# Kernel tuning notes

Measured on AMD Instinct MI355X. Metric: run time of the kernel, lower is better.

Reference implementation:

```python
import jax, jax.numpy as jnp
import numpy as np

EPS = 1e-5  # BatchNorm2d default eps


def setup_inputs() -> dict:
    key = jax.random.key(0)
    k1, k2, k3, k4 = jax.random.split(key, 4)
    B, C, S, E = 2, 512, 256, 512  # C == E is required by the module's math
    x = jax.random.normal(k1, (B, C, S, E), dtype=jnp.float32)
    Q = jax.random.normal(k2, (E, E), dtype=jnp.float32)
    K = jax.random.normal(k3, (E, E), dtype=jnp.float32)
    V = jax.random.normal(k4, (E, E), dtype=jnp.float32)
    return {"x": x, "Q": Q, "K": K, "V": V}


def reference(x, Q, K, V):
    # BatchNorm2d(affine=False), training-mode batch stats over (B, H, W)
    mean = jnp.mean(x, axis=(0, 2, 3), keepdims=True)
    var = jnp.var(x, axis=(0, 2, 3), keepdims=True)  # biased, matches torch normalization
    xn = (x - mean) * jax.lax.rsqrt(var + EPS)

    divisor = jnp.sqrt(jnp.asarray(x.shape[-1], dtype=x.dtype))
    q = jnp.einsum('bcse,ef->bcsf', xn, Q)
    k = jnp.einsum('bcse,ef->bcsf', xn, K)
    v = jnp.einsum('bcse,ef->bcsf', xn, V)

    # scores: [B, C, S, S]
    prod = jnp.einsum('bcsf,bctf->bcst', q, k) / divisor
    # nn.Softmax2d softmaxes over the CHANNEL dim (axis 1)
    sm = jax.nn.softmax(prod, axis=1)
    attention = jnp.einsum('bcst,bctf->bcsf', sm, v)
    # dropout is identity in eval/reference mode; residual since E_in == E_out
    return attention + xn
```

## Files before the change

### kernel.cpp

```cpp
#include <hip/hip_runtime.h>
#include <hip/hip_bf16.h>
#include <cstdio>

#define Bn 2
#define Cn 512
#define Sn 256
#define En 512

typedef __attribute__((ext_vector_type(8))) short bf16x8;
typedef __attribute__((ext_vector_type(4))) float f32x4;

static constexpr size_t PROD_B = (1ull << 20);
static constexpr size_t V_B    = PROD_B + (256ull << 20);
static constexpr size_t ATH_B  = V_B + (256ull << 20);
static constexpr size_t ATL_B  = ATH_B + (512ull << 10);
static constexpr size_t VT_B   = ATL_B + (512ull << 10);
static constexpr size_t WS_SMALL = VT_B + (512ull << 10);
static constexpr size_t XNH_B  = WS_SMALL;
static constexpr size_t XNL_B  = XNH_B + (256ull << 20);
static constexpr size_t WS_BIG = XNL_B + (256ull << 20);

__device__ __forceinline__ unsigned short f2bf(float f) {
  union { __hip_bfloat16 h; unsigned short u; } cv;
  cv.h = __float2bfloat16(f);
  return cv.u;
}
__device__ __forceinline__ float bf2f(unsigned short u) {
  union { unsigned int i; float f; } cv;
  cv.i = ((unsigned int)u) << 16;
  return cv.f;
}
__device__ __forceinline__ void split2(float v, unsigned short& h, unsigned short& l) {
  h = f2bf(v);
  l = f2bf(v - bf2f(h));
}
__device__ __forceinline__ int swz8(int row, int c4) {
  return row * 64 + ((((c4 * 8) ^ ((row & 7) << 4))) >> 1);
}
__device__ __forceinline__ int swzc(int row, int col) {
  return row * 64 + ((col & 3) | ((col & 60) ^ ((row & 7) << 3)));
}
__device__ __forceinline__ bf16x8 ldfrag(const unsigned short* arr, int row, int ks, int lane) {
  const int byte = (ks * 64 + ((lane >> 4) << 4)) ^ ((row & 7) << 4);
  return *(const bf16x8*)((const char*)(arr + (size_t)row * 64) + byte);
}
__device__ __forceinline__ f32x4 MFMA(bf16x8 a, bf16x8 b, f32x4 c) {
  return __builtin_amdgcn_mfma_f32_16x16x32_bf16(a, b, c, 0, 0, 0);
}
__device__ __forceinline__ void glds16(const void* g, void* l) {
  __builtin_amdgcn_global_load_lds(
      (const __attribute__((address_space(1))) unsigned int*)g,
      (__attribute__((address_space(3))) unsigned int*)l, 16, 0, 0);
}
__device__ __forceinline__ void stage_tile(const unsigned short* g, unsigned short* l,
                                           int nbytes, int wid, int lane, int nwaves) {
  const char* gb = (const char*)g;
  char* lb = (char*)l;
  for (int j = wid; j < (nbytes >> 10); j += nwaves)
    glds16(gb + j * 1024 + lane * 16, lb + j * 1024);
}

__global__ void k1_stats(const float* __restrict__ x, float* __restrict__ ws) {
  const int c = blockIdx.x, tid = threadIdx.x;
  const float4* p0 = (const float4*)(x + (size_t)c * (Sn * En));
  const float4* p1 = (const float4*)(x + (size_t)(Cn + c) * (Sn * En));
  float s1 = 0.f, s2 = 0.f;
  for (int i = tid; i < (Sn * En / 4); i += 256) {
    float4 a = p0[i], b = p1[i];
    s1 += (a.x + a.y) + (a.z + a.w) + (b.x + b.y) + (b.z + b.w);
    s2 += (a.x * a.x + a.y * a.y) + (a.z * a.z + a.w * a.w) +
          (b.x * b.x + b.y * b.y) + (b.z * b.z + b.w * b.w);
  }
  __shared__ float r1[256], r2[256];
  r1[tid] = s1; r2[tid] = s2;
  __syncthreads();
  for (int off = 128; off > 0; off >>= 1) {
    if (tid < off) { r1[tid] += r1[tid + off]; r2[tid] += r2[tid + off]; }
    __syncthreads();
  }
  if (tid == 0) {
    const float n = (float)(2 * Sn * En);
    float mean = r1[0] / n;
    float var = r2[0] / n - mean * mean;
    ws[c] = mean;
    ws[512 + c] = 1.0f / sqrtf(var + 1e-5f);
  }
}

__global__ void kA(const float* __restrict__ Q, const float* __restrict__ K,
                   const float* __restrict__ V, unsigned short* __restrict__ ATh,
                   unsigned short* __restrict__ ATl, unsigned short* __restrict__ VT) {
  const int f = blockIdx.x, tid = threadIdx.x;
  __shared__ float Kf[512];
  for (int i = tid; i < 512; i += 256) Kf[i] = K[(size_t)f * 512 + i];
  __syncthreads();
  const int fr64 = f & 63;
  const size_t atbase = ((size_t)(f >> 6) * 8) * 4096 + (size_t)fr64 * 64;
  const size_t vtbase = ((size_t)(f >> 7) * 8) * 8192 + (size_t)(f & 127) * 64;
#pragma unroll
  for (int half = 0; half < 2; ++half) {
    const int e = tid + half * 256;
    const float* Qe = Q + (size_t)e * 512;
    float acc = 0.f;
    for (int t = 0; t < 512; t += 4) {
      float4 q = *(const float4*)(Qe + t);
      acc += q.x * Kf[t] + q.y * Kf[t + 1] + q.z * Kf[t + 2] + q.w * Kf[t + 3];
    }
    unsigned short h, l;
    split2(acc, h, l);
    const int et = e >> 6, ec = e & 63;
    const int swa = (ec & 3) | ((ec & 60) ^ ((fr64 & 7) << 3));
    ATh[atbase + (size_t)et * 4096 + swa] = h;
    ATl[atbase + (size_t)et * 4096 + swa] = l;
    const int swv = (ec & 3) | ((ec & 60) ^ ((f & 7) << 3));
    VT[vtbase + (size_t)et * 8192 + swv] = f2bf(V[(size_t)e * 512 + f]);
  }
}

__global__ void kxn(const float* __restrict__ x, const float* __restrict__ ws,
                    unsigned short* __restrict__ XNh, unsigned short* __restrict__ XNl) {
  const int bid = blockIdx.x;
  const int bc = bid >> 1, half = bid & 1;
  const int c = bc & 511;
  const float mean = ws[c], rstd = ws[512 + c];
  const float* xb = x + (size_t)bc * 131072 + (size_t)half * 128 * 512;
  const int tid = threadIdx.x;
#pragma unroll 4
  for (int i = 0; i < 64; ++i) {
    const int g = tid + i * 256;
    const int r = g >> 7, c4 = g & 127;
    const float4 xv = *(const float4*)(xb + (size_t)r * 512 + c4 * 4);
    ushort4 hv, lv;
    split2((xv.x - mean) * rstd, hv.x, lv.x);
    split2((xv.y - mean) * rstd, hv.y, lv.y);
    split2((xv.z - mean) * rstd, hv.z, lv.z);
    split2((xv.w - mean) * rstd, hv.w, lv.w);
    const int et = c4 >> 4, colt4 = c4 & 15;
    const int row = half * 128 + r;
    const size_t idx = ((size_t)(bc * 8 + et) * 256 + row) * 64 +
                       ((colt4 * 4) ^ ((row & 7) << 3));
    *(ushort4*)&XNh[idx] = hv;
    *(ushort4*)&XNl[idx] = lv;
  }
}

template <bool PRE>
__launch_bounds__(256)
__global__ void kv_proj(const float* __restrict__ x, const unsigned short* __restrict__ VT,
                        const unsigned short* __restrict__ XNh_g,
                        const float* __restrict__ ws, unsigned short* __restrict__ vT_out) {
  __shared__ unsigned short VTs[128 * 64];
  __shared__ unsigned short XN[128 * 64];
  const int bid = blockIdx.x;
  const int L = (bid & 7) * 1024 + (bid >> 3);
  const int bc = L >> 3;
  const int fq = (L >> 1) & 3;
  const int th = L & 1;
  const int c = bc & 511;
  const float mean = ws[c], rstd = ws[512 + c];
  const int f0 = fq * 128, t0 = th * 128;
  const int tid = threadIdx.x, w = tid >> 6, lane = tid & 63;
  const float* xb = x + (size_t)bc * 131072;

  f32x4 acc[2][8];
#pragma unroll
  for (int i = 0; i < 2; ++i)
#pragma unroll
    for (int j = 0; j < 8; ++j) acc[i][j] = (f32x4){0.f, 0.f, 0.f, 0.f};

  for (int et = 0; et < 8; ++et) {
    const int e0 = et * 64;
    __syncthreads();
    stage_tile(VT + ((size_t)fq * 8 + et) * 8192, VTs, 16384, w, lane, 4);
    if (PRE) {
      stage_tile(XNh_g + ((size_t)(bc * 8 + et) * 256 + t0) * 64, XN, 16384, w, lane, 4);
    } else {
#pragma unroll
      for (int i = 0; i < 8; ++i) {
        const int g = tid + i * 256;
        const int r = g >> 4, c4 = g & 15;
        float4 xv = *(const float4*)(xb + (size_t)(t0 + r) * 512 + e0 + c4 * 4);
        ushort4 hv;
        hv.x = f2bf((xv.x - mean) * rstd);
        hv.y = f2bf((xv.y - mean) * rstd);
        hv.z = f2bf((xv.z - mean) * rstd);
        hv.w = f2bf((xv.w - mean) * rstd);
        *(ushort4*)&XN[swz8(r, c4)] = hv;
      }
    }
    __syncthreads();
#pragma unroll
    for (int ks = 0; ks < 2; ++ks) {
      bf16x8 a0 = ldfrag(VTs, w * 32 + (lane & 15), ks, lane);
      bf16x8 a1 = ldfrag(VTs, w * 32 + 16 + (lane & 15), ks, lane);
#pragma unroll
      for (int ct = 0; ct < 8; ++ct) {
        bf16x8 b = ldfrag(XN, ct * 16 + (lane & 15), ks, lane);
        acc[0][ct] = MFMA(a0, b, acc[0][ct]);
        acc[1][ct] = MFMA(a1, b, acc[1][ct]);
      }
    }
  }
#pragma unroll
  for (int rt = 0; rt < 2; ++rt)
#pragma unroll
    for (int ct = 0; ct < 8; ++ct)
#pragma unroll
      for (int r = 0; r < 4; ++r) {
        const int f = f0 + w * 32 + rt * 16 + (lane >> 4) * 4 + r;
        const int t = t0 + ct * 16 + (lane & 15);
        const size_t idx = (((size_t)bc * 4 + (f >> 7)) * 4 + (t >> 6)) * 8192 +
                           (size_t)(f & 127) * 64 +
                           ((t & 3) | ((t & 60) ^ ((f & 7) << 3)));
        vT_out[idx] = f2bf(acc[rt][ct][r]);
      }
}

template <bool PRE>
__launch_bounds__(512)
__global__ void kscores(const float* __restrict__ x, const unsigned short* __restrict__ ATh_g,
                        const unsigned short* __restrict__ ATl_g,
                        const unsigned short* __restrict__ XNh_g,
                        const unsigned short* __restrict__ XNl_g,
                        const float* __restrict__ ws, float* __restrict__ prod) {
  __shared__ unsigned short XNh[128 * 64], XNl[128 * 64];
  __shared__ unsigned short ATh[64 * 64], ATl[64 * 64];
  __shared__ unsigned short Yh[128 * 64], Yl[128 * 64];
  const int bid = blockIdx.x;
  const int L = (bid & 7) * 256 + (bid >> 3);
  const int bc = L >> 1, half = L & 1;
  const int c = bc & 511;
  const float mean = ws[c], rstd = ws[512 + c];
  const float* xc = x + (size_t)bc * (Sn * En);
  const float* xr = xc + (size_t)half * 128 * 512;
  float* prodc = prod + (size_t)bc * 65536 + (size_t)half * 128 * 256;
  const int tid = threadIdx.x, w = tid >> 6, lane = tid & 63;

  f32x4 accz[16];
#pragma unroll
  for (int i = 0; i < 16; ++i) accz[i] = (f32x4){0.f, 0.f, 0.f, 0.f};

  for (int ft = 0; ft < 8; ++ft) {
    const int f0 = ft * 64;
    f32x4 accy[4];
#pragma unroll
    for (int i = 0; i < 4; ++i) accy[i] = (f32x4){0.f, 0.f, 0.f, 0.f};

    for (int et = 0; et < 8; ++et) {
      const int e0 = et * 64;
      __syncthreads();
      if (PRE) {
        stage_tile(XNh_g + ((size_t)(bc * 8 + et) * 256 + half * 128) * 64, XNh,
                   16384, w, lane, 8);
        stage_tile(XNl_g + ((size_t)(bc * 8 + et) * 256 + half * 128) * 64, XNl,
                   16384, w, lane, 8);
      } else {
#pragma unroll
        for (int i = 0; i < 4; ++i) {
          const int g = tid + i * 512;
          const int r = g >> 4, c4 = g & 15;
          float4 xv = *(const float4*)(xr + (size_t)r * 512 + e0 + c4 * 4);
          ushort4 hv, lv;
          split2((xv.x - mean) * rstd, hv.x, lv.x);
          split2((xv.y - mean) * rstd, hv.y, lv.y);
          split2((xv.z - mean) * rstd, hv.z, lv.z);
          split2((xv.w - mean) * rstd, hv.w, lv.w);
          *(ushort4*)&XNh[swz8(r, c4)] = hv;
          *(ushort4*)&XNl[swz8(r, c4)] = lv;
        }
      }
      stage_tile(ATh_g + ((size_t)ft * 8 + et) * 4096, ATh, 8192, w, lane, 8);
      stage_tile(ATl_g + ((size_t)ft * 8 + et) * 4096, ATl, 8192, w, lane, 8);
      __syncthreads();
#pragma unroll
      for (int ks = 0; ks < 2; ++ks) {
        bf16x8 ah = ldfrag(XNh, w * 16 + (lane & 15), ks, lane);
        bf16x8 al = ldfrag(XNl, w * 16 + (lane & 15), ks, lane);
#pragma unroll
        for (int fc = 0; fc < 4; ++fc) {
          bf16x8 bh = ldfrag(ATh, fc * 16 + (lane & 15), ks, lane);
          bf16x8 bl = ldfrag(ATl, fc * 16 + (lane & 15), ks, lane);
          accy[fc] = MFMA(ah, bh, accy[fc]);
          accy[fc] = MFMA(ah, bl, accy[fc]);
          accy[fc] = MFMA(al, bh, accy[fc]);
        }
      }
    }
    __syncthreads();

#pragma unroll
    for (int fc = 0; fc < 4; ++fc)
#pragma unroll
      for (int r = 0; r < 4; ++r) {
        const int row = w * 16 + (lane >> 4) * 4 + r;
        const int col = fc * 16 + (lane & 15);
        unsigned short h, l;
        split2(accy[fc][r], h, l);
        const int idx = swzc(row, col);
        Yh[idx] = h;
        Yl[idx] = l;
      }
#pragma unroll
    for (int th = 0; th < 2; ++th) {
      if (PRE) {
        stage_tile(XNh_g + ((size_t)(bc * 8 + ft) * 256 + th * 128) * 64, XNh,
                   16384, w, lane, 8);
        stage_tile(XNl_g + ((size_t)(bc * 8 + ft) * 256 + th * 128) * 64, XNl,
                   16384, w, lane, 8);
      } else {
#pragma unroll
        for (int i = 0; i < 4; ++i) {
          const int g = tid + i * 512;
          const int r = g >> 4, c4 = g & 15;
          float4 xv = *(const float4*)(xc + (size_t)(th * 128 + r) * 512 + f0 + c4 * 4);
          ushort4 hv, lv;
          split2((xv.x - mean) * rstd, hv.x, lv.x);
          split2((xv.y - mean) * rstd, hv.y, lv.y);
          split2((xv.z - mean) * rstd, hv.z, lv.z);
          split2((xv.w - mean) * rstd, hv.w, lv.w);
          *(ushort4*)&XNh[swz8(r, c4)] = hv;
          *(ushort4*)&XNl[swz8(r, c4)] = lv;
        }
      }
      __syncthreads();
#pragma unroll
      for (int ks = 0; ks < 2; ++ks) {
        bf16x8 ah = ldfrag(Yh, w * 16 + (lane & 15), ks, lane);
        bf16x8 al = ldfrag(Yl, w * 16 + (lane & 15), ks, lane);
#pragma unroll
        for (int ct = 0; ct < 8; ++ct) {
          bf16x8 bh = ldfrag(XNh, ct * 16 + (lane & 15), ks, lane);
          bf16x8 bl = ldfrag(XNl, ct * 16 + (lane & 15), ks, lane);
          accz[th * 8 + ct] = MFMA(ah, bh, accz[th * 8 + ct]);
          accz[th * 8 + ct] = MFMA(ah, bl, accz[th * 8 + ct]);
          accz[th * 8 + ct] = MFMA(al, bh, accz[th * 8 + ct]);
        }
      }
      __syncthreads();
    }
  }
  const float scale = 0.044194173824159216f;
#pragma unroll
  for (int th = 0; th < 2; ++th)
#pragma unroll
    for (int ct = 0; ct < 8; ++ct)
#pragma unroll
      for (int r = 0; r < 4; ++r) {
        const int row = w * 16 + (lane >> 4) * 4 + r;
        prodc[(size_t)row * 256 + th * 128 + ct * 16 + (lane & 15)] =
            accz[th * 8 + ct][r] * scale;
      }
}

__global__ void k3_softmax(float* __restrict__ prodf) {
  const int bid = blockIdx.x;
  const int b = bid >> 8, s = bid & 255;
  const int t = threadIdx.x;
  float* __restrict__ p = prodf + (size_t)b * (512ull * 65536) + (size_t)s * 256 + t;
  float m = -3.4e38f, sum = 0.f;
#pragma unroll 8
  for (int cc = 0; cc < 512; ++cc) {
    const float v = p[(size_t)cc * 65536];
    if (v > m) { sum *= __expf(m - v); m = v; }
    sum += __expf(v - m);
  }
  const float inv = 1.0f / sum;
#pragma unroll 4
  for (int cc = 0; cc < 512; ++cc) {
    p[(size_t)cc * 65536] = __expf(p[(size_t)cc * 65536] - m) * inv;
  }
}

__launch_bounds__(256)
__global__ void k4_pv(const float* __restrict__ x, const unsigned short* __restrict__ vT,
                      const float* __restrict__ ws, const float* __restrict__ sm,
                      float* __restrict__ out) {
  __shared__ unsigned short SMs[128 * 64];
  __shared__ unsigned short VTs[128 * 64];
  const int bid = blockIdx.x;
  const int L = (bid & 7) * 1024 + (bid >> 3);
  const int bc = L >> 3;
  const int sh = (L >> 2) & 1;
  const int fh = L & 3;
  const int c = bc & 511;
  const float mean = ws[c], rstd = ws[512 + c];
  const int s0 = sh * 128, f0 = fh * 128;
  const float* smb = sm + (size_t)bc * 65536;
  const int tid = threadIdx.x, w = tid >> 6, lane = tid & 63;

  f32x4 acc[2][8];
#pragma unroll
  for (int i = 0; i < 2; ++i)
#pragma unroll
    for (int j = 0; j < 8; ++j) acc[i][j] = (f32x4){0.f, 0.f, 0.f, 0.f};

  for (int kt = 0; kt < 4; ++kt) {
    const int t0 = kt * 64;
    __syncthreads();
    stage_tile(vT + (((size_t)bc * 4 + fh) * 4 + kt) * 8192, VTs, 16384, w, lane, 4);
#pragma unroll
    for (int i = 0; i < 8; ++i) {
      const int g = tid + i * 256;
      const int r = g >> 4, c4 = g & 15;
      float4 pv = *(const float4*)(smb + (size_t)(s0 + r) * 256 + t0 + c4 * 4);
      ushort4 hv;
      hv.x = f2bf(pv.x); hv.y = f2bf(pv.y); hv.z = f2bf(pv.z); hv.w = f2bf(pv.w);
      *(ushort4*)&SMs[swz8(r, c4)] = hv;
    }
    __syncthreads();
#pragma unroll
    for (int ks = 0; ks < 2; ++ks) {
      bf16x8 a0 = ldfrag(SMs, w * 32 + (lane & 15), ks, lane);
      bf16x8 a1 = ldfrag(SMs, w * 32 + 16 + (lane & 15), ks, lane);
#pragma unroll
      for (int ct = 0; ct < 8; ++ct) {
        bf16x8 b = ldfrag(VTs, ct * 16 + (lane & 15), ks, lane);
        acc[0][ct] = MFMA(a0, b, acc[0][ct]);
        acc[1][ct] = MFMA(a1, b, acc[1][ct]);
      }
    }
  }
#pragma unroll
  for (int rt = 0; rt < 2; ++rt)
#pragma unroll
    for (int ct = 0; ct < 8; ++ct)
#pragma unroll
      for (int r = 0; r < 4; ++r) {
        const int srow = s0 + w * 32 + rt * 16 + (lane >> 4) * 4 + r;
        const int fcol = f0 + ct * 16 + (lane & 15);
        const size_t oi = (size_t)bc * 131072 + (size_t)srow * 512 + fcol;
        out[oi] = acc[rt][ct][r] + (x[oi] - mean) * rstd;
      }
}

extern "C" void kernel_launch(void* const* d_in, const int* in_sizes, int n_in,
                              void* d_out, int out_size, void* d_ws, size_t ws_size,
                              hipStream_t stream) {
  const float* x = (const float*)d_in[0];
  const float* Q = (const float*)d_in[1];
  const float* K = (const float*)d_in[2];
  const float* V = (const float*)d_in[3];
  float* out = (float*)d_out;
  float* ws = (float*)d_ws;
  float* prodf = (float*)((char*)d_ws + PROD_B);
  unsigned short* vT   = (unsigned short*)((char*)d_ws + V_B);
  unsigned short* ATh  = (unsigned short*)((char*)d_ws + ATH_B);
  unsigned short* ATl  = (unsigned short*)((char*)d_ws + ATL_B);
  unsigned short* VTm  = (unsigned short*)((char*)d_ws + VT_B);
  unsigned short* XNh  = (unsigned short*)((char*)d_ws + XNH_B);
  unsigned short* XNl  = (unsigned short*)((char*)d_ws + XNL_B);
  if (ws_size < WS_SMALL) {
    fprintf(stderr, "kernel_launch: ws_size %zu < needed %zu\n", ws_size, WS_SMALL);
  }
  const bool big = ws_size >= WS_BIG;
  k1_stats<<<dim3(512), dim3(256), 0, stream>>>(x, ws);
  kA<<<dim3(512), dim3(256), 0, stream>>>(Q, K, V, ATh, ATl, VTm);
  if (big) {
    kxn<<<dim3(2048), dim3(256), 0, stream>>>(x, ws, XNh, XNl);
    kv_proj<true><<<dim3(8192), dim3(256), 0, stream>>>(x, VTm, XNh, ws, vT);
    kscores<true><<<dim3(2048), dim3(512), 0, stream>>>(x, ATh, ATl, XNh, XNl, ws, prodf);
  } else {
    kv_proj<false><<<dim3(8192), dim3(256), 0, stream>>>(x, VTm, XNh, ws, vT);
    kscores<false><<<dim3(2048), dim3(512), 0, stream>>>(x, ATh, ATl, XNh, XNl, ws, prodf);
  }
  k3_softmax<<<dim3(512), dim3(256), 0, stream>>>(prodf);
  k4_pv<<<dim3(8192), dim3(256), 0, stream>>>(x, vT, ws, prodf, out);
}
```

Before: 2.107 ms.

## Double-buffer LDS staging in GEMM kernels and emit bf16 tiled softmax output

kv_proj, kscores and k4_pv now double-buffer their LDS tiles, so the async global-to-LDS load for the next k-step overlaps the MFMAs on the current one, with one barrier per step. kscores flattens its nested loops into a single 80-step schedule so this prefetch can run across phases. Softmax splits the 512-channel reduction over two thread halves and writes bf16 probabilities straight into the swizzled tile layout that k4_pv reads, so k4_pv no longer reads and converts fp32. The non-precomputed fallback is dropped, so the code now always needs the large workspace and the smT buffer reuses the XNl region.

```diff
diff --git a/kernel.cpp b/kernel.cpp
--- a/kernel.cpp
+++ b/kernel.cpp
@@ -15,10 +15,10 @@
 static constexpr size_t ATH_B  = V_B + (256ull << 20);
 static constexpr size_t ATL_B  = ATH_B + (512ull << 10);
 static constexpr size_t VT_B   = ATL_B + (512ull << 10);
-static constexpr size_t WS_SMALL = VT_B + (512ull << 10);
-static constexpr size_t XNH_B  = WS_SMALL;
+static constexpr size_t XNH_B  = VT_B + (512ull << 10);
 static constexpr size_t XNL_B  = XNH_B + (256ull << 20);
 static constexpr size_t WS_BIG = XNL_B + (256ull << 20);
+static constexpr size_t SMT_B  = XNL_B;
 
 __device__ __forceinline__ unsigned short f2bf(float f) {
   union { __hip_bfloat16 h; unsigned short u; } cv;
@@ -33,9 +33,6 @@
 __device__ __forceinline__ void split2(float v, unsigned short& h, unsigned short& l) {
   h = f2bf(v);
   l = f2bf(v - bf2f(h));
-}
-__device__ __forceinline__ int swz8(int row, int c4) {
-  return row * 64 + ((((c4 * 8) ^ ((row & 7) << 4))) >> 1);
 }
 __device__ __forceinline__ int swzc(int row, int col) {
   return row * 64 + ((col & 3) | ((col & 60) ^ ((row & 7) << 3)));
@@ -144,23 +141,18 @@
   }
 }
 
-template <bool PRE>
 __launch_bounds__(256)
-__global__ void kv_proj(const float* __restrict__ x, const unsigned short* __restrict__ VT,
+__global__ void kv_proj(const unsigned short* __restrict__ VT,
                         const unsigned short* __restrict__ XNh_g,
-                        const float* __restrict__ ws, unsigned short* __restrict__ vT_out) {
-  __shared__ unsigned short VTs[128 * 64];
-  __shared__ unsigned short XN[128 * 64];
+                        unsigned short* __restrict__ vT_out) {
+  __shared__ unsigned short BUF[2][16384];
   const int bid = blockIdx.x;
   const int L = (bid & 7) * 1024 + (bid >> 3);
   const int bc = L >> 3;
   const int fq = (L >> 1) & 3;
   const int th = L & 1;
-  const int c = bc & 511;
-  const float mean = ws[c], rstd = ws[512 + c];
   const int f0 = fq * 128, t0 = th * 128;
   const int tid = threadIdx.x, w = tid >> 6, lane = tid & 63;
-  const float* xb = x + (size_t)bc * 131072;
 
   f32x4 acc[2][8];
 #pragma unroll
@@ -168,38 +160,30 @@
 #pragma unroll
     for (int j = 0; j < 8; ++j) acc[i][j] = (f32x4){0.f, 0.f, 0.f, 0.f};
 
+  stage_tile(VT + ((size_t)fq * 8 + 0) * 8192, &BUF[0][0], 16384, w, lane, 4);
+  stage_tile(XNh_g + ((size_t)(bc * 8 + 0) * 256 + t0) * 64, &BUF[0][8192], 16384, w, lane, 4);
+  __syncthreads();
+#pragma unroll 1
   for (int et = 0; et < 8; ++et) {
-    const int e0 = et * 64;
-    __syncthreads();
-    stage_tile(VT + ((size_t)fq * 8 + et) * 8192, VTs, 16384, w, lane, 4);
-    if (PRE) {
-      stage_tile(XNh_g + ((size_t)(bc * 8 + et) * 256 + t0) * 64, XN, 16384, w, lane, 4);
-    } else {
-#pragma unroll
-      for (int i = 0; i < 8; ++i) {
-        const int g = tid + i * 256;
-        const int r = g >> 4, c4 = g & 15;
-        float4 xv = *(const float4*)(xb + (size_t)(t0 + r) * 512 + e0 + c4 * 4);
-        ushort4 hv;
-        hv.x = f2bf((xv.x - mean) * rstd);
-        hv.y = f2bf((xv.y - mean) * rstd);
-        hv.z = f2bf((xv.z - mean) * rstd);
-        hv.w = f2bf((xv.w - mean) * rstd);
-        *(ushort4*)&XN[swz8(r, c4)] = hv;
-      }
-    }
-    __syncthreads();
+    if (et < 7) {
+      const int b = (et + 1) & 1;
+      stage_tile(VT + ((size_t)fq * 8 + et + 1) * 8192, &BUF[b][0], 16384, w, lane, 4);
+      stage_tile(XNh_g + ((size_t)(bc * 8 + et + 1) * 256 + t0) * 64, &BUF[b][8192],
+                 16384, w, lane, 4);
+    }
+    const unsigned short* cb = &BUF[et & 1][0];
 #pragma unroll
     for (int ks = 0; ks < 2; ++ks) {
-      bf16x8 a0 = ldfrag(VTs, w * 32 + (lane & 15), ks, lane);
-      bf16x8 a1 = ldfrag(VTs, w * 32 + 16 + (lane & 15), ks, lane);
+      bf16x8 a0 = ldfrag(cb, w * 32 + (lane & 15), ks, lane);
+      bf16x8 a1 = ldfrag(cb, w * 32 + 16 + (lane & 15), ks, lane);
 #pragma unroll
       for (int ct = 0; ct < 8; ++ct) {
-        bf16x8 b = ldfrag(XN, ct * 16 + (lane & 15), ks, lane);
+        bf16x8 b = ldfrag(cb + 8192, ct * 16 + (lane & 15), ks, lane);
         acc[0][ct] = MFMA(a0, b, acc[0][ct]);
         acc[1][ct] = MFMA(a1, b, acc[1][ct]);
       }
     }
+    __syncthreads();
   }
 #pragma unroll
   for (int rt = 0; rt < 2; ++rt)
@@ -216,129 +200,116 @@
       }
 }
 
-template <bool PRE>
 __launch_bounds__(512)
-__global__ void kscores(const float* __restrict__ x, const unsigned short* __restrict__ ATh_g,
+__global__ void kscores(const unsigned short* __restrict__ ATh_g,
                         const unsigned short* __restrict__ ATl_g,
                         const unsigned short* __restrict__ XNh_g,
                         const unsigned short* __restrict__ XNl_g,
-                        const float* __restrict__ ws, float* __restrict__ prod) {
-  __shared__ unsigned short XNh[128 * 64], XNl[128 * 64];
-  __shared__ unsigned short ATh[64 * 64], ATl[64 * 64];
+                        float* __restrict__ prod) {
+  __shared__ unsigned short BUF[2][24576];
   __shared__ unsigned short Yh[128 * 64], Yl[128 * 64];
   const int bid = blockIdx.x;
   const int L = (bid & 7) * 256 + (bid >> 3);
   const int bc = L >> 1, half = L & 1;
-  const int c = bc & 511;
-  const float mean = ws[c], rstd = ws[512 + c];
-  const float* xc = x + (size_t)bc * (Sn * En);
-  const float* xr = xc + (size_t)half * 128 * 512;
   float* prodc = prod + (size_t)bc * 65536 + (size_t)half * 128 * 256;
   const int tid = threadIdx.x, w = tid >> 6, lane = tid & 63;
 
   f32x4 accz[16];
 #pragma unroll
   for (int i = 0; i < 16; ++i) accz[i] = (f32x4){0.f, 0.f, 0.f, 0.f};
-
-  for (int ft = 0; ft < 8; ++ft) {
-    const int f0 = ft * 64;
-    f32x4 accy[4];
-#pragma unroll
-    for (int i = 0; i < 4; ++i) accy[i] = (f32x4){0.f, 0.f, 0.f, 0.f};
-
-    for (int et = 0; et < 8; ++et) {
-      const int e0 = et * 64;
-      __syncthreads();
-      if (PRE) {
-        stage_tile(XNh_g + ((size_t)(bc * 8 + et) * 256 + half * 128) * 64, XNh,
-                   16384, w, lane, 8);
-        stage_tile(XNl_g + ((size_t)(bc * 8 + et) * 256 + half * 128) * 64, XNl,
-                   16384, w, lane, 8);
-      } else {
-#pragma unroll
-        for (int i = 0; i < 4; ++i) {
-          const int g = tid + i * 512;
-          const int r = g >> 4, c4 = g & 15;
-          float4 xv = *(const float4*)(xr + (size_t)r * 512 + e0 + c4 * 4);
-          ushort4 hv, lv;
-          split2((xv.x - mean) * rstd, hv.x, lv.x);
-          split2((xv.y - mean) * rstd, hv.y, lv.y);
-          split2((xv.z - mean) * rstd, hv.z, lv.z);
-          split2((xv.w - mean) * rstd, hv.w, lv.w);
-          *(ushort4*)&XNh[swz8(r, c4)] = hv;
-          *(ushort4*)&XNl[swz8(r, c4)] = lv;
-        }
-      }
-      stage_tile(ATh_g + ((size_t)ft * 8 + et) * 4096, ATh, 8192, w, lane, 8);
-      stage_tile(ATl_g + ((size_t)ft * 8 + et) * 4096, ATl, 8192, w, lane, 8);
-      __syncthreads();
+  f32x4 accy[4];
+
+  auto stage_slot = [&](int m, int b) {
+    const int ft = m / 10, sub = m - ft * 10;
+    unsigned short* dst = &BUF[b][0];
+    if (sub < 8) {
+      stage_tile(XNh_g + ((size_t)(bc * 8 + sub) * 256 + half * 128) * 64, dst,
+                 16384, w, lane, 8);
+      stage_tile(XNl_g + ((size_t)(bc * 8 + sub) * 256 + half * 128) * 64, dst + 8192,
+                 16384, w, lane, 8);
+      stage_tile(ATh_g + ((size_t)ft * 8 + sub) * 4096, dst + 16384, 8192, w, lane, 8);
+      stage_tile(ATl_g + ((size_t)ft * 8 + sub) * 4096, dst + 20480, 8192, w, lane, 8);
+    } else {
+      const int th = sub - 8;
+      stage_tile(XNh_g + ((size_t)(bc * 8 + ft) * 256 + th * 128) * 64, dst,
+                 16384, w, lane, 8);
+      stage_tile(XNl_g + ((size_t)(bc * 8 + ft) * 256 + th * 128) * 64, dst + 8192,
+                 16384, w, lane, 8);
+    }
+  };
+
+  stage_slot(0, 0);
+  __syncthreads();
+
+#pragma unroll 1
+  for (int m = 0; m < 80; ++m) {
+    const int sub = m % 10;
+    if (m < 79) stage_slot(m + 1, (m + 1) & 1);
+    const unsigned short* cb = &BUF[m & 1][0];
+    if (sub == 0) {
+#pragma unroll
+      for (int i = 0; i < 4; ++i) accy[i] = (f32x4){0.f, 0.f, 0.f, 0.f};
+    }
+    if (sub < 8) {
 #pragma unroll
       for (int ks = 0; ks < 2; ++ks) {
-        bf16x8 ah = ldfrag(XNh, w * 16 + (lane & 15), ks, lane);
-        bf16x8 al = ldfrag(XNl, w * 16 + (lane & 15), ks, lane);
+        bf16x8 ah = ldfrag(cb, w * 16 + (lane & 15), ks, lane);
+        bf16x8 al = ldfrag(cb + 8192, w * 16 + (lane & 15), ks, lane);
 #pragma unroll
         for (int fc = 0; fc < 4; ++fc) {
-          bf16x8 bh = ldfrag(ATh, fc * 16 + (lane & 15), ks, lane);
-          bf16x8 bl = ldfrag(ATl, fc * 16 + (lane & 15), ks, lane);
+          bf16x8 bh = ldfrag(cb + 16384, fc * 16 + (lane & 15), ks, lane);
+          bf16x8 bl = ldfrag(cb + 20480, fc * 16 + (lane & 15), ks, lane);
           accy[fc] = MFMA(ah, bh, accy[fc]);
           accy[fc] = MFMA(ah, bl, accy[fc]);
           accy[fc] = MFMA(al, bh, accy[fc]);
         }
       }
-    }
-    __syncthreads();
-
-#pragma unroll
-    for (int fc = 0; fc < 4; ++fc)
-#pragma unroll
-      for (int r = 0; r < 4; ++r) {
-        const int row = w * 16 + (lane >> 4) * 4 + r;
-        const int col = fc * 16 + (lane & 15);
-        unsigned short h, l;
-        split2(accy[fc][r], h, l);
-        const int idx = swzc(row, col);
-        Yh[idx] = h;
-        Yl[idx] = l;
-      }
-#pragma unroll
-    for (int th = 0; th < 2; ++th) {
-      if (PRE) {
-        stage_tile(XNh_g + ((size_t)(bc * 8 + ft) * 256 + th * 128) * 64, XNh,
-                   16384, w, lane, 8);
-        stage_tile(XNl_g + ((size_t)(bc * 8 + ft) * 256 + th * 128) * 64, XNl,
-                   16384, w, lane, 8);
-      } else {
-#pragma unroll
-        for (int i = 0; i < 4; ++i) {
-          const int g = tid + i * 512;
-          const int r = g >> 4, c4 = g & 15;
-          float4 xv = *(const float4*)(xc + (size_t)(th * 128 + r) * 512 + f0 + c4 * 4);
-          ushort4 hv, lv;
-          split2((xv.x - mean) * rstd, hv.x, lv.x);
-          split2((xv.y - mean) * rstd, hv.y, lv.y);
-          split2((xv.z - mean) * rstd, hv.z, lv.z);
-          split2((xv.w - mean) * rstd, hv.w, lv.w);
-          *(ushort4*)&XNh[swz8(r, c4)] = hv;
-          *(ushort4*)&XNl[swz8(r, c4)] = lv;
-        }
-      }
-      __syncthreads();
+      if (sub == 7) {
+#pragma unroll
+        for (int fc = 0; fc < 4; ++fc)
+#pragma unroll
+          for (int r = 0; r < 4; ++r) {
+            const int row = w * 16 + (lane >> 4) * 4 + r;
+            const int col = fc * 16 + (lane & 15);
+            unsigned short h, l;
+            split2(accy[fc][r], h, l);
+            const int idx = swzc(row, col);
+            Yh[idx] = h;
+            Yl[idx] = l;
+          }
+      }
+    } else if (sub == 8) {
 #pragma unroll
       for (int ks = 0; ks < 2; ++ks) {
         bf16x8 ah = ldfrag(Yh, w * 16 + (lane & 15), ks, lane);
         bf16x8 al = ldfrag(Yl, w * 16 + (lane & 15), ks, lane);
 #pragma unroll
         for (int ct = 0; ct < 8; ++ct) {
-          bf16x8 bh = ldfrag(XNh, ct * 16 + (lane & 15), ks, lane);
-          bf16x8 bl = ldfrag(XNl, ct * 16 + (lane & 15), ks, lane);
-          accz[th * 8 + ct] = MFMA(ah, bh, accz[th * 8 + ct]);
-          accz[th * 8 + ct] = MFMA(ah, bl, accz[th * 8 + ct]);
-          accz[th * 8 + ct] = MFMA(al, bh, accz[th * 8 + ct]);
+          bf16x8 bh = ldfrag(cb, ct * 16 + (lane & 15), ks, lane);
+          bf16x8 bl = ldfrag(cb + 8192, ct * 16 + (lane & 15), ks, lane);
+          accz[ct] = MFMA(ah, bh, accz[ct]);
+          accz[ct] = MFMA(ah, bl, accz[ct]);
+          accz[ct] = MFMA(al, bh, accz[ct]);
         }
       }
-      __syncthreads();
-    }
-  }
+    } else {
+#pragma unroll
+      for (int ks = 0; ks < 2; ++ks) {
+        bf16x8 ah = ldfrag(Yh, w * 16 + (lane & 15), ks, lane);
+        bf16x8 al = ldfrag(Yl, w * 16 + (lane & 15), ks, lane);
+#pragma unroll
+        for (int ct = 0; ct < 8; ++ct) {
+          bf16x8 bh = ldfrag(cb, ct * 16 + (lane & 15), ks, lane);
+          bf16x8 bl = ldfrag(cb + 8192, ct * 16 + (lane & 15), ks, lane);
+          accz[8 + ct] = MFMA(ah, bh, accz[8 + ct]);
+          accz[8 + ct] = MFMA(ah, bl, accz[8 + ct]);
+          accz[8 + ct] = MFMA(al, bh, accz[8 + ct]);
+        }
+      }
+    }
+    __syncthreads();
+  }
+
   const float scale = 0.044194173824159216f;
 #pragma unroll
   for (int th = 0; th < 2; ++th)
@@ -352,31 +323,42 @@
       }
 }
 
-__global__ void k3_softmax(float* __restrict__ prodf) {
+__launch_bounds__(512)
+__global__ void k3_softmax(const float* __restrict__ prodf, unsigned short* __restrict__ smT) {
   const int bid = blockIdx.x;
   const int b = bid >> 8, s = bid & 255;
-  const int t = threadIdx.x;
-  float* __restrict__ p = prodf + (size_t)b * (512ull * 65536) + (size_t)s * 256 + t;
+  const int tid = threadIdx.x;
+  const int t = tid & 255, ch = tid >> 8;
+  const float* __restrict__ p =
+      prodf + (size_t)b * (512ull * 65536) + (size_t)s * 256 + t + (size_t)ch * 256 * 65536;
   float m = -3.4e38f, sum = 0.f;
-#pragma unroll 8
-  for (int cc = 0; cc < 512; ++cc) {
+#pragma unroll 4
+  for (int cc = 0; cc < 256; ++cc) {
     const float v = p[(size_t)cc * 65536];
     if (v > m) { sum *= __expf(m - v); m = v; }
     sum += __expf(v - m);
   }
-  const float inv = 1.0f / sum;
+  __shared__ float Ms[2][256], Ss[2][256];
+  Ms[ch][t] = m; Ss[ch][t] = sum;
+  __syncthreads();
+  const float mo = Ms[ch ^ 1][t], so = Ss[ch ^ 1][t];
+  const float mm = fmaxf(m, mo);
+  const float inv = 1.0f / (sum * __expf(m - mm) + so * __expf(mo - mm));
+  const int sh = s >> 7, r = s & 127, kt = t >> 6, col = t & 63;
+  const int cidx = r * 64 + ((col & 3) | ((col & 60) ^ ((r & 7) << 3)));
+  const size_t tbase = ((size_t)b * 512 + ch * 256) * 2 + sh;
 #pragma unroll 4
-  for (int cc = 0; cc < 512; ++cc) {
-    p[(size_t)cc * 65536] = __expf(p[(size_t)cc * 65536] - m) * inv;
+  for (int cc = 0; cc < 256; ++cc) {
+    const float ev = __expf(p[(size_t)cc * 65536] - mm) * inv;
+    smT[((tbase + (size_t)cc * 2) * 4 + kt) * 8192 + cidx] = f2bf(ev);
   }
 }
 
 __launch_bounds__(256)
 __global__ void k4_pv(const float* __restrict__ x, const unsigned short* __restrict__ vT,
-                      const float* __restrict__ ws, const float* __restrict__ sm,
+                      const float* __restrict__ ws, const unsigned short* __restrict__ smT,
                       float* __restrict__ out) {
-  __shared__ unsigned short SMs[128 * 64];
-  __shared__ unsigned short VTs[128 * 64];
+  __shared__ unsigned short BUF[2][16384];
   const int bid = blockIdx.x;
   const int L = (bid & 7) * 1024 + (bid >> 3);
   const int bc = L >> 3;
@@ -385,7 +367,6 @@
   const int c = bc & 511;
   const float mean = ws[c], rstd = ws[512 + c];
   const int s0 = sh * 128, f0 = fh * 128;
-  const float* smb = sm + (size_t)bc * 65536;
   const int tid = threadIdx.x, w = tid >> 6, lane = tid & 63;
 
   f32x4 acc[2][8];
@@ -394,31 +375,31 @@
 #pragma unroll
     for (int j = 0; j < 8; ++j) acc[i][j] = (f32x4){0.f, 0.f, 0.f, 0.f};
 
+  stage_tile(smT + (((size_t)bc * 2 + sh) * 4 + 0) * 8192, &BUF[0][0], 16384, w, lane, 4);
+  stage_tile(vT + (((size_t)bc * 4 + fh) * 4 + 0) * 8192, &BUF[0][8192], 16384, w, lane, 4);
+  __syncthreads();
+#pragma unroll 1
   for (int kt = 0; kt < 4; ++kt) {
-    const int t0 = kt * 64;
-    __syncthreads();
-    stage_tile(vT + (((size_t)bc * 4 + fh) * 4 + kt) * 8192, VTs, 16384, w, lane, 4);
-#pragma unroll
-    for (int i = 0; i < 8; ++i) {
-      const int g = tid + i * 256;
-      const int r = g >> 4, c4 = g & 15;
-      float4 pv = *(const float4*)(smb + (size_t)(s0 + r) * 256 + t0 + c4 * 4);
-      ushort4 hv;
-      hv.x = f2bf(pv.x); hv.y = f2bf(pv.y); hv.z = f2bf(pv.z); hv.w = f2bf(pv.w);
-      *(ushort4*)&SMs[swz8(r, c4)] = hv;
-    }
-    __syncthreads();
+    if (kt < 3) {
+      const int b = (kt + 1) & 1;
+      stage_tile(smT + (((size_t)bc * 2 + sh) * 4 + kt + 1) * 8192, &BUF[b][0],
+                 16384, w, lane, 4);
+      stage_tile(vT + (((size_t)bc * 4 + fh) * 4 + kt + 1) * 8192, &BUF[b][8192],
+                 16384, w, lane, 4);
+    }
+    const unsigned short* cb = &BUF[kt & 1][0];
 #pragma unroll
     for (int ks = 0; ks < 2; ++ks) {
-      bf16x8 a0 = ldfrag(SMs, w * 32 + (lane & 15), ks, lane);
-      bf16x8 a1 = ldfrag(SMs, w * 32 + 16 + (lane & 15), ks, lane);
+      bf16x8 a0 = ldfrag(cb, w * 32 + (lane & 15), ks, lane);
+      bf16x8 a1 = ldfrag(cb, w * 32 + 16 + (lane & 15), ks, lane);
 #pragma unroll
       for (int ct = 0; ct < 8; ++ct) {
-        bf16x8 b = ldfrag(VTs, ct * 16 + (lane & 15), ks, lane);
+        bf16x8 b = ldfrag(cb + 8192, ct * 16 + (lane & 15), ks, lane);
         acc[0][ct] = MFMA(a0, b, acc[0][ct]);
         acc[1][ct] = MFMA(a1, b, acc[1][ct]);
       }
     }
+    __syncthreads();
   }
 #pragma unroll
   for (int rt = 0; rt < 2; ++rt)
@@ -449,20 +430,16 @@
   unsigned short* VTm  = (unsigned short*)((char*)d_ws + VT_B);
   unsigned short* XNh  = (unsigned short*)((char*)d_ws + XNH_B);
   unsigned short* XNl  = (unsigned short*)((char*)d_ws + XNL_B);
-  if (ws_size < WS_SMALL) {
-    fprintf(stderr, "kernel_launch: ws_size %zu < needed %zu\n", ws_size, WS_SMALL);
-  }
-  const bool big = ws_size >= WS_BIG;
+  unsigned short* smT  = (unsigned short*)((char*)d_ws + SMT_B);
+  if (ws_size < WS_BIG) {
+    fprintf(stderr, "kernel_launch: ws_size %zu < needed %zu — expect corruption\n",
+            ws_size, WS_BIG);
+  }
   k1_stats<<<dim3(512), dim3(256), 0, stream>>>(x, ws);
   kA<<<dim3(512), dim3(256), 0, stream>>>(Q, K, V, ATh, ATl, VTm);
-  if (big) {
-    kxn<<<dim3(2048), dim3(256), 0, stream>>>(x, ws, XNh, XNl);
-    kv_proj<true><<<dim3(8192), dim3(256), 0, stream>>>(x, VTm, XNh, ws, vT);
-    kscores<true><<<dim3(2048), dim3(512), 0, stream>>>(x, ATh, ATl, XNh, XNl, ws, prodf);
-  } else {
-    kv_proj<false><<<dim3(8192), dim3(256), 0, stream>>>(x, VTm, XNh, ws, vT);
-    kscores<false><<<dim3(2048), dim3(512), 0, stream>>>(x, ATh, ATl, XNh, XNl, ws, prodf);
-  }
-  k3_softmax<<<dim3(512), dim3(256), 0, stream>>>(prodf);
-  k4_pv<<<dim3(8192), dim3(256), 0, stream>>>(x, vT, ws, prodf, out);
-}
+  kxn<<<dim3(2048), dim3(256), 0, stream>>>(x, ws, XNh, XNl);
+  kv_proj<<<dim3(8192), dim3(256), 0, stream>>>(VTm, XNh, vT);
+  kscores<<<dim3(2048), dim3(512), 0, stream>>>(ATh, ATl, XNh, XNl, prodf);
+  k3_softmax<<<dim3(512), dim3(512), 0, stream>>>(prodf, smT);
+  k4_pv<<<dim3(8192), dim3(256), 0, stream>>>(x, vT, ws, smT, out);
+}
```

Result: no change. 2.076 ms (-1.5%).
